# Kernel tuning notes

Hardware: AMD Instinct MI355X
Metric: run time of the kernel (lower is better)

Reference implementation:

```python
import jax, jax.numpy as jnp
import numpy as np
import itertools

B, G, FEAT, IMG = 2048, 8, 512, 1024
SCALES = list(range(G, 1, -1))  # [8,7,6,5,4,3,2]
SUBSAMPLE = 12


def setup_inputs() -> dict:
    key = jax.random.key(0)
    keys = jax.random.split(key, 1 + 2 * len(SCALES))
    rng = np.random.default_rng(0)
    inp = {"input": jax.random.normal(keys[0], (B, G, FEAT), dtype=jnp.float32)}
    for i, scale in enumerate(SCALES):
        perms = np.array(list(itertools.permutations(range(G), scale)), dtype=np.int32)
        n_sub = min(SUBSAMPLE, len(perms))
        sel = rng.choice(len(perms), n_sub, replace=False)
        inp[f"perms{i}"] = jnp.asarray(perms[sel])  # [n_sub, scale] int32
        lim = 1.0 / np.sqrt(scale * FEAT)
        inp[f"W{i}"] = jax.random.uniform(keys[1 + 2 * i], (IMG, scale * FEAT), minval=-lim, maxval=lim, dtype=jnp.float32)
        inp[f"b{i}"] = jax.random.uniform(keys[2 + 2 * i], (IMG,), minval=-lim, maxval=lim, dtype=jnp.float32)
    return inp


def _forward(input, perms_list, W_list, b_list):
    outs = []
    for perms, W, b in zip(perms_list, W_list, b_list):
        # gather: [B, n_sub, scale, FEAT] -> [B, n_sub, scale*FEAT]
        g = input[:, perms, :]
        g = g.reshape(g.shape[0], g.shape[1], -1)
        # batched linear over all subsamples, then mean over subsamples
        y = jnp.einsum('bsf,df->bsd', g, W) + b  # [B, n_sub, IMG]
        outs.append(y.mean(axis=1))
    return jnp.concatenate(outs, axis=1)  # [B, len(SCALES)*IMG]


def reference(input, perms0, W0, b0, perms1, W1, b1, perms2, W2, b2,
              perms3, W3, b3, perms4, W4, b4, perms5, W5, b5, perms6, W6, b6):
    perms_list = [perms0, perms1, perms2, perms3, perms4, perms5, perms6]
    W_list = [W0, W1, W2, W3, W4, W5, W6]
    b_list = [b0, b1, b2, b3, b4, b5, b6]
    return _forward(input, perms_list, W_list, b_list)
```

## Files before the change

### kernel.cpp

```cpp
#include <hip/hip_runtime.h>

typedef unsigned short u16;
typedef __bf16 bf16x8 __attribute__((ext_vector_type(8)));
typedef float f32x4 __attribute__((ext_vector_type(4)));

__device__ __forceinline__ u16 f2bf(float f) {
  unsigned int u = __float_as_uint(f);
  return (u16)((u + 0x7fffu + ((u >> 16) & 1u)) >> 16);
}

__device__ __forceinline__ int cumK(int i) { return 256 * i * (17 - i); }

__global__ __launch_bounds__(256) void k_xbar(
    const float* __restrict__ x,
    const int* p0, const int* p1, const int* p2, const int* p3,
    const int* p4, const int* p5, const int* p6,
    u16* __restrict__ Xb) {
  __shared__ float sc[448];
  const int b = blockIdx.x;
  const int t = threadIdx.x;
  const int* ps[7] = {p0, p1, p2, p3, p4, p5, p6};
  for (int cell = t; cell < 448; cell += 256) {
    int i = cell >> 6, rem = cell & 63, g = rem >> 3, j = rem & 7;
    int scale = 8 - i;
    float v = 0.f;
    if (j < scale) {
      const int* p = ps[i];
      int cnt = 0;
      for (int s = 0; s < 12; ++s) cnt += (p[s * scale + j] == g) ? 1 : 0;
      v = (float)cnt * (1.0f / 12.0f);
    }
    sc[cell] = v;
  }
  __syncthreads();
  const int u = t & 63;
  const int wv = t >> 6;
  const float4* xrow = reinterpret_cast<const float4*>(x + (size_t)b * 4096);
  float4 xr0[8], xr1[8];
#pragma unroll
  for (int g = 0; g < 8; ++g) {
    xr0[g] = xrow[g * 128 + u * 2];
    xr1[g] = xrow[g * 128 + u * 2 + 1];
  }
  u16* orow = Xb + (size_t)b * 17920;
  for (int s = wv; s < 35; s += 4) {
    int i = 0, rem = s;
    while (rem >= 8 - i) { rem -= 8 - i; ++i; }
    const int j = rem;
    float4 A0 = make_float4(0.f, 0.f, 0.f, 0.f);
    float4 A1 = make_float4(0.f, 0.f, 0.f, 0.f);
#pragma unroll
    for (int g = 0; g < 8; ++g) {
      const float c = sc[i * 64 + g * 8 + j];
      A0.x += c * xr0[g].x; A0.y += c * xr0[g].y;
      A0.z += c * xr0[g].z; A0.w += c * xr0[g].w;
      A1.x += c * xr1[g].x; A1.y += c * xr1[g].y;
      A1.z += c * xr1[g].z; A1.w += c * xr1[g].w;
    }
    uint4 o;
    o.x = (unsigned)f2bf(A0.x) | ((unsigned)f2bf(A0.y) << 16);
    o.y = (unsigned)f2bf(A0.z) | ((unsigned)f2bf(A0.w) << 16);
    o.z = (unsigned)f2bf(A1.x) | ((unsigned)f2bf(A1.y) << 16);
    o.w = (unsigned)f2bf(A1.z) | ((unsigned)f2bf(A1.w) << 16);
    *reinterpret_cast<uint4*>(orow + cumK(i) + j * 512 + u * 8) = o;
  }
}

__global__ __launch_bounds__(256) void k_wcast(
    const float* W0, const float* W1, const float* W2, const float* W3,
    const float* W4, const float* W5, const float* W6,
    u16* __restrict__ Wcat) {
  int i = 0, rem = blockIdx.x;
  while (rem >= (8 - i) * 512) { rem -= (8 - i) * 512; ++i; }
  const float* Wi = (i == 0) ? W0 : (i == 1) ? W1 : (i == 2) ? W2 :
                    (i == 3) ? W3 : (i == 4) ? W4 : (i == 5) ? W5 : W6;
  const int t = threadIdx.x;
  const float4 w = reinterpret_cast<const float4*>(Wi)[(size_t)rem * 256 + t];
  ushort4 o;
  o.x = f2bf(w.x); o.y = f2bf(w.y); o.z = f2bf(w.z); o.w = f2bf(w.w);
  reinterpret_cast<ushort4*>(Wcat + ((size_t)cumK(i) + rem) * 1024)[t] = o;
}

__device__ __forceinline__ void gl_lds16(const u16* g, u16* l) {
  __builtin_amdgcn_global_load_lds(
      (const __attribute__((address_space(1))) void*)g,
      (__attribute__((address_space(3))) void*)l, 16, 0, 0);
}

__global__ __launch_bounds__(256) void k_gemm_ms(
    const u16* __restrict__ Xb, const u16* __restrict__ Wcat,
    const float* b0, const float* b1, const float* b2, const float* b3,
    const float* b4, const float* b5, const float* b6,
    float* __restrict__ out) {
  __shared__ u16 sA[128 * 64];
  __shared__ u16 sB[128 * 64];
  const int r = blockIdx.x >> 7;
  const int i = (r == 0) ? 0 : (r == 1) ? 1 : (r == 2) ? 4 :
                (r == 3) ? 2 : (r == 4) ? 5 : (r == 5) ? 3 : 6;
  const int s = blockIdx.x & 127;
  const int m0 = (s >> 3) * 128;
  const int n0loc = (s & 7) * 128;
  const int K = (8 - i) * 512;
  const int niter = K >> 6;
  const size_t baseB = (size_t)cumK(i) * 1024;

  const int tid = threadIdx.x;
  const int lane = tid & 63;
  const int wave = tid >> 6;
  const int quad = lane >> 4;
  const int l15 = lane & 15;
  const int waveM = (wave >> 1) * 64;
  const int waveN = (wave & 1) * 64;

  const int srow = tid >> 3;
  const int sslot = tid & 7;
  const int gch = (sslot - srow) & 7;
  const u16* pA0 = Xb + (size_t)(m0 + srow) * 17920 + cumK(i) + gch * 8;
  const u16* pB0 = Wcat + baseB + (size_t)(n0loc + srow) * K + gch * 8;
  u16* lA0 = sA + tid * 8;
  u16* lB0 = sB + tid * 8;
  const size_t strideAj = (size_t)32 * 17920;
  const size_t strideBj = (size_t)32 * K;

  int offA[2][4], offB[2][4];
#pragma unroll
  for (int t = 0; t < 2; ++t) {
#pragma unroll
    for (int q = 0; q < 4; ++q) {
      int rowA = waveM + q * 16 + l15;
      offA[t][q] = rowA * 64 + (((t * 4 + quad) + rowA) & 7) * 8;
      int rowB = waveN + q * 16 + l15;
      offB[t][q] = rowB * 64 + (((t * 4 + quad) + rowB) & 7) * 8;
    }
  }

  f32x4 acc[4][4];
#pragma unroll
  for (int q = 0; q < 4; ++q)
#pragma unroll
    for (int c = 0; c < 4; ++c) {
      f32x4 z = {0.f, 0.f, 0.f, 0.f};
      acc[q][c] = z;
    }

  for (int kt = 0; kt < niter; ++kt) {
    const size_t ko = (size_t)kt * 64;
#pragma unroll
    for (int j = 0; j < 4; ++j) {
      gl_lds16(pA0 + j * strideAj + ko, lA0 + j * 2048);
      gl_lds16(pB0 + j * strideBj + ko, lB0 + j * 2048);
    }
    __syncthreads();

#pragma unroll
    for (int t = 0; t < 2; ++t) {
      bf16x8 av[4], bv[4];
#pragma unroll
      for (int q = 0; q < 4; ++q) av[q] = *reinterpret_cast<const bf16x8*>(sA + offA[t][q]);
#pragma unroll
      for (int c = 0; c < 4; ++c) bv[c] = *reinterpret_cast<const bf16x8*>(sB + offB[t][c]);
#pragma unroll
      for (int q = 0; q < 4; ++q)
#pragma unroll
        for (int c = 0; c < 4; ++c)
          acc[q][c] = __builtin_amdgcn_mfma_f32_16x16x32_bf16(av[q], bv[c], acc[q][c], 0, 0, 0);
    }
    __syncthreads();
  }

  const float* bi = (i == 0) ? b0 : (i == 1) ? b1 : (i == 2) ? b2 :
                    (i == 3) ? b3 : (i == 4) ? b4 : (i == 5) ? b5 : b6;
#pragma unroll
  for (int c = 0; c < 4; ++c) {
    const int nloc = n0loc + waveN + c * 16 + l15;
    const float bias = bi[nloc];
    const int ncol = i * 1024 + nloc;
#pragma unroll
    for (int q = 0; q < 4; ++q) {
      const int mbase = m0 + waveM + q * 16 + quad * 4;
#pragma unroll
      for (int reg = 0; reg < 4; ++reg)
        out[(size_t)(mbase + reg) * 7168 + ncol] = acc[q][c][reg] + bias;
    }
  }
}

extern "C" void kernel_launch(void* const* d_in, const int* in_sizes, int n_in,
                              void* d_out, int out_size, void* d_ws, size_t ws_size,
                              hipStream_t stream) {
  const float* input = (const float*)d_in[0];
  const int* perms[7];
  const float* W[7];
  const float* bias[7];
  for (int i = 0; i < 7; ++i) {
    perms[i] = (const int*)d_in[1 + 3 * i];
    W[i]     = (const float*)d_in[2 + 3 * i];
    bias[i]  = (const float*)d_in[3 + 3 * i];
  }
  char* ws = (char*)d_ws;
  u16* Xb   = (u16*)ws;
  u16* Wcat = (u16*)(ws + (size_t)2048 * 17920 * 2);

  k_xbar<<<2048, 256, 0, stream>>>(input, perms[0], perms[1], perms[2], perms[3],
                                   perms[4], perms[5], perms[6], Xb);
  k_wcast<<<17920, 256, 0, stream>>>(W[0], W[1], W[2], W[3], W[4], W[5], W[6], Wcat);
  k_gemm_ms<<<896, 256, 0, stream>>>(Xb, Wcat,
                                     bias[0], bias[1], bias[2], bias[3],
                                     bias[4], bias[5], bias[6],
                                     (float*)d_out);
}
```

Measured before the change: 321.5 us.

## Double-buffer LDS tiles in GEMM and remap block order for locality

The GEMM main loop now keeps two LDS buffers. It issues the async global-to-LDS loads for the next K tile before computing on the current one, and uses explicit vmcnt waits plus raw barriers in place of full __syncthreads. This is meant to overlap memory latency with MFMA work. Block scheduling also changes: the scale-interleaving order is dropped, and tiles are remapped so neighbouring blocks share A/B rows within 4x4 groups, which should improve L2 reuse. LDS use doubles to 64KB, which can lower occupancy, and the hand-written waitcnt encodings have to be correct for the target.

```diff
diff --git a/kernel.cpp b/kernel.cpp
--- a/kernel.cpp
+++ b/kernel.cpp
@@ -87,19 +87,23 @@
       (__attribute__((address_space(3))) void*)l, 16, 0, 0);
 }
 
+#define WAIT_VM8 0x0F78
+#define WAIT_VM0 0x0F70
+
 __global__ __launch_bounds__(256) void k_gemm_ms(
     const u16* __restrict__ Xb, const u16* __restrict__ Wcat,
     const float* b0, const float* b1, const float* b2, const float* b3,
     const float* b4, const float* b5, const float* b6,
     float* __restrict__ out) {
-  __shared__ u16 sA[128 * 64];
-  __shared__ u16 sB[128 * 64];
-  const int r = blockIdx.x >> 7;
-  const int i = (r == 0) ? 0 : (r == 1) ? 1 : (r == 2) ? 4 :
-                (r == 3) ? 2 : (r == 4) ? 5 : (r == 5) ? 3 : 6;
+  __shared__ u16 lds[2 * 16384];
+  const int i = blockIdx.x >> 7;
   const int s = blockIdx.x & 127;
-  const int m0 = (s >> 3) * 128;
-  const int n0loc = (s & 7) * 128;
+  const int region = s & 7;
+  const int k = s >> 3;
+  const int mq = region >> 1;
+  const int nq = region & 1;
+  const int m0 = (mq * 4 + (k & 3)) * 128;
+  const int n0loc = (nq * 4 + (k >> 2)) * 128;
   const int K = (8 - i) * 512;
   const int niter = K >> 6;
   const size_t baseB = (size_t)cumK(i) * 1024;
@@ -117,10 +121,10 @@
   const int gch = (sslot - srow) & 7;
   const u16* pA0 = Xb + (size_t)(m0 + srow) * 17920 + cumK(i) + gch * 8;
   const u16* pB0 = Wcat + baseB + (size_t)(n0loc + srow) * K + gch * 8;
-  u16* lA0 = sA + tid * 8;
-  u16* lB0 = sB + tid * 8;
   const size_t strideAj = (size_t)32 * 17920;
   const size_t strideBj = (size_t)32 * K;
+  u16* lA0 = lds + tid * 8;
+  u16* lB0 = lds + 8192 + tid * 8;
 
   int offA[2][4], offB[2][4];
 #pragma unroll
@@ -130,7 +134,7 @@
       int rowA = waveM + q * 16 + l15;
       offA[t][q] = rowA * 64 + (((t * 4 + quad) + rowA) & 7) * 8;
       int rowB = waveN + q * 16 + l15;
-      offB[t][q] = rowB * 64 + (((t * 4 + quad) + rowB) & 7) * 8;
+      offB[t][q] = 8192 + rowB * 64 + (((t * 4 + quad) + rowB) & 7) * 8;
     }
   }
 
@@ -143,29 +147,56 @@
       acc[q][c] = z;
     }
 
-  for (int kt = 0; kt < niter; ++kt) {
-    const size_t ko = (size_t)kt * 64;
+#pragma unroll
+  for (int j = 0; j < 4; ++j) {
+    gl_lds16(pA0 + j * strideAj, lA0 + j * 2048);
+    gl_lds16(pB0 + j * strideBj, lB0 + j * 2048);
+  }
+
+  for (int kt = 0; kt < niter - 1; ++kt) {
+    const size_t ko = (size_t)(kt + 1) * 64;
+    const int nb = ((kt + 1) & 1) << 14;
 #pragma unroll
     for (int j = 0; j < 4; ++j) {
-      gl_lds16(pA0 + j * strideAj + ko, lA0 + j * 2048);
-      gl_lds16(pB0 + j * strideBj + ko, lB0 + j * 2048);
-    }
-    __syncthreads();
-
+      gl_lds16(pA0 + j * strideAj + ko, lA0 + nb + j * 2048);
+      gl_lds16(pB0 + j * strideBj + ko, lB0 + nb + j * 2048);
+    }
+    __builtin_amdgcn_s_waitcnt(WAIT_VM8);
+    __builtin_amdgcn_s_barrier();
+    const int boff = (kt & 1) << 14;
 #pragma unroll
     for (int t = 0; t < 2; ++t) {
       bf16x8 av[4], bv[4];
 #pragma unroll
-      for (int q = 0; q < 4; ++q) av[q] = *reinterpret_cast<const bf16x8*>(sA + offA[t][q]);
-#pragma unroll
-      for (int c = 0; c < 4; ++c) bv[c] = *reinterpret_cast<const bf16x8*>(sB + offB[t][c]);
+      for (int q = 0; q < 4; ++q) av[q] = *reinterpret_cast<const bf16x8*>(lds + boff + offA[t][q]);
+#pragma unroll
+      for (int c = 0; c < 4; ++c) bv[c] = *reinterpret_cast<const bf16x8*>(lds + boff + offB[t][c]);
 #pragma unroll
       for (int q = 0; q < 4; ++q)
 #pragma unroll
         for (int c = 0; c < 4; ++c)
           acc[q][c] = __builtin_amdgcn_mfma_f32_16x16x32_bf16(av[q], bv[c], acc[q][c], 0, 0, 0);
     }
-    __syncthreads();
+    __builtin_amdgcn_s_barrier();
+  }
+
+  __builtin_amdgcn_s_waitcnt(WAIT_VM0);
+  __builtin_amdgcn_s_barrier();
+  {
+    const int boff = ((niter - 1) & 1) << 14;
+#pragma unroll
+    for (int t = 0; t < 2; ++t) {
+      bf16x8 av[4], bv[4];
+#pragma unroll
+      for (int q = 0; q < 4; ++q) av[q] = *reinterpret_cast<const bf16x8*>(lds + boff + offA[t][q]);
+#pragma unroll
+      for (int c = 0; c < 4; ++c) bv[c] = *reinterpret_cast<const bf16x8*>(lds + boff + offB[t][c]);
+#pragma unroll
+      for (int q = 0; q < 4; ++q)
+#pragma unroll
+        for (int c = 0; c < 4; ++c)
+          acc[q][c] = __builtin_amdgcn_mfma_f32_16x16x32_bf16(av[q], bv[c], acc[q][c], 0, 0, 0);
+    }
   }
 
   const float* bi = (i == 0) ? b0 : (i == 1) ? b1 : (i == 2) ? b2 :
```

Result: faster. 279.0 us (-13.2%).
